# Kernel tuning notes

Hardware: AMD Instinct MI355X
Metric: run time of the kernel (lower is better)

The kernel has to match this reference:

```python
import jax, jax.numpy as jnp
import numpy as np

R_CUT = 10.0
ROUNDS = 1  # num_message_passing_rounds


def setup_inputs() -> dict:
    key = jax.random.key(0)
    N, DEG, S, NRBF, G = 10000, 16, 128, 20, 64
    E = N * DEG
    ks = jax.random.split(key, 16)
    w = lambda k, shp, fan: (jax.random.normal(k, shp, dtype=jnp.float32) / np.float32(np.sqrt(fan)))
    return {
        "edge_vector_diffs": jax.random.normal(ks[0], (E, 3), dtype=jnp.float32) * 3.0,
        "edge_lengths": jax.random.uniform(ks[1], (E,), dtype=jnp.float32) * 15.0,
        "node_from": jnp.repeat(jnp.arange(N), DEG),            # every node has DEG outgoing edges
        "node_graph_index": jax.random.randint(ks[2], (N,), 0, G),
        "num_graphs": G,
        "emb0": jax.random.normal(ks[3], (S,), dtype=jnp.float32) * 0.01,  # embedding.weight[0]
        "phi_w1": w(ks[4], (S, S), S), "phi_b1": jnp.zeros((S,), jnp.float32),
        "phi_w2": w(ks[5], (S, 3 * S), S), "phi_b2": jnp.zeros((3 * S,), jnp.float32),
        "filt_w": w(ks[6], (NRBF, 3 * S), NRBF), "filt_b": jnp.zeros((3 * S,), jnp.float32),
        "u_w": w(ks[7], (S, S), S), "v_w": w(ks[8], (S, S), S),
        "upd_w1": w(ks[9], (2 * S, S), 2 * S), "upd_b1": jnp.zeros((S,), jnp.float32),
        "upd_w2": w(ks[10], (S, 3 * S), S), "upd_b2": jnp.zeros((3 * S,), jnp.float32),
        "out_w1": w(ks[11], (S, S), S), "out_b1": jnp.zeros((S,), jnp.float32),
        "out_w2": w(ks[12], (S, 1), S), "out_b2": jnp.zeros((1,), jnp.float32),
    }


def reference(edge_vector_diffs, edge_lengths, node_from, node_graph_index, num_graphs,
              emb0, phi_w1, phi_b1, phi_w2, phi_b2, filt_w, filt_b, u_w, v_w,
              upd_w1, upd_b1, upd_w2, upd_b2, out_w1, out_b1, out_w2, out_b2):
    S = phi_w1.shape[0]
    N = node_graph_index.shape[0]
    NRBF = filt_w.shape[0]
    silu = jax.nn.silu
    seg = lambda v, n: jax.ops.segment_sum(v, node_from, num_segments=n)

    mask = (jnp.abs(edge_lengths) <= R_CUT).astype(jnp.float32)          # [E] nbr_mask
    r = jnp.linalg.norm(edge_vector_diffs, axis=1)                        # [E]
    r_safe = jnp.maximum(r, 1e-12)
    k = jnp.arange(1, NRBF + 1, dtype=jnp.float32)
    # PAINN sinc radial basis sin(k*pi*r/r_cut)/r, then linear -> [E, 3S]
    rbf = jnp.sin(k[None, :] * jnp.pi * r_safe[:, None] / R_CUT) / r_safe[:, None]
    cutoff = 0.5 * (jnp.cos(jnp.pi * r / R_CUT) + 1.0) * (r < R_CUT)      # cosine cutoff
    W = (rbf @ filt_w + filt_b) * cutoff[:, None]                          # [E, 3S]

    tile3 = jnp.arange(S) % 3  # xyzxyz... truncation pattern from .repeat(...)[: S]
    # scalar Frobenius norm of each node's masked neighbor-diff block
    frob = jnp.sqrt(seg(mask * r * r, N))                                  # [N]
    denom_e = frob[node_from]
    denom_e = jnp.where(denom_e > 0, denom_e, 1.0)
    normalized = edge_vector_diffs / denom_e[:, None]                      # [E, 3]
    norm_exp = normalized[:, tile3]                                        # [E, S]

    # state init: sum over dim 1 of embedding(zeros) == S * embedding.weight[0]
    state = jnp.broadcast_to(jnp.float32(S) * emb0, (N, S))
    state_vec = jnp.zeros((N, 3, S), jnp.float32)

    for _ in range(ROUNDS):
        # message block (nbrs_node_from == destination node, so sync update == original sequential loop)
        phi = silu(state[node_from] @ phi_w1 + phi_b1) @ phi_w2 + phi_b2   # [E, 3S]
        prod = phi * W
        m1, m2, m3 = prod[:, :S], prod[:, S:2 * S], prod[:, 2 * S:]
        vec_msg = state_vec[node_from] * m1[:, None, :] + (norm_exp * m3)[:, None, :]  # [E,3,S]
        state = seg(m2 * mask[:, None], N)                                 # [N, S]
        state_vec = seg(vec_msg * mask[:, None, None], N)                  # [N, 3, S]
        # update block
        U = jnp.einsum('nps,st->npt', state_vec, u_w)                      # [N,3,S]
        V = jnp.einsum('nps,st->npt', state_vec, v_w)
        UV = jnp.einsum('nps,nqs->npq', U, V)                              # [N,3,3]
        Vnorm = jnp.sqrt(jnp.sum(V * V, axis=1))                           # [N,S]
        a = silu(jnp.concatenate([Vnorm, state], axis=-1) @ upd_w1 + upd_b1) @ upd_w2 + upd_b2
        a_vv, a_sv, a_ss = a[:, :S], a[:, S:2 * S], a[:, 2 * S:]
        uv_tiled = jnp.sum(UV, axis=1)[:, tile3]                           # [N,S]
        state = a_ss + uv_tiled * a_sv
        state_vec = U * a_vv[:, None, :]

    graph_state = jax.ops.segment_sum(state, node_graph_index, num_segments=num_graphs)
    out = (silu(graph_state @ out_w1 + out_b1) @ out_w2 + out_b2).ravel()  # [num_graphs]
    return out
```

## Files before the change

### kernel.cpp

```cpp
#include <hip/hip_runtime.h>
#include <math.h>

#define NN   10000
#define DEG  16
#define SS   128
#define NRBF 20
#define GG   64
#define RC   10.0f
#define PI_F 3.14159265358979323846f
#define NB   4

__device__ __forceinline__ float silu_f(float x){
    return x / (1.0f + __expf(-x));
}

__global__ __launch_bounds__(128) void k_phi(
    const float* __restrict__ emb0,
    const float* __restrict__ w1, const float* __restrict__ b1,
    const float* __restrict__ w2, const float* __restrict__ b2,
    float* __restrict__ phiW){
    __shared__ float s0[SS];
    __shared__ float hL[SS];
    __shared__ float part[2][4];
    int t = threadIdx.x, bid = blockIdx.x;
    s0[t] = 128.0f * emb0[t];
    __syncthreads();
    float acc = 0.0f;
    #pragma unroll 8
    for (int s = 0; s < SS; s++)
        acc = fmaf(s0[s], w1[s*SS + t], acc);
    hL[t] = silu_f(acc + b1[t]);
    __syncthreads();
    int c0 = bid * 4;
    float4 wq = *((const float4*)(w2 + t*3*SS + c0));
    float h = hL[t];
    float p[4] = {h*wq.x, h*wq.y, h*wq.z, h*wq.w};
    int lane = t & 63, wid = t >> 6;
    #pragma unroll
    for (int j = 0; j < 4; j++){
        float v = p[j];
        for (int off = 32; off; off >>= 1) v += __shfl_down(v, off);
        if (lane == 0) part[wid][j] = v;
    }
    __syncthreads();
    if (t < 4) phiW[c0 + t] = b2[c0 + t] + part[0][t] + part[1][t];
}

__global__ __launch_bounds__(128) void k_node(
    const float* __restrict__ evd, const float* __restrict__ elen,
    const float* __restrict__ filt_w, const float* __restrict__ filt_b,
    const float* __restrict__ phiW,
    const float* __restrict__ u_w, const float* __restrict__ v_w,
    const float* __restrict__ upd_w1, const float* __restrict__ upd_b1,
    const float* __restrict__ upd_w2, const float* __restrict__ upd_b2,
    const int* __restrict__ ngi, float* __restrict__ gs){
    __shared__ float rS[NB*DEG];
    __shared__ float mcL[NB*DEG];
    __shared__ float frL[NB*DEG];
    __shared__ float eV[NB*DEG][3];
    __shared__ float rbfL[NB*DEG][NRBF];
    __shared__ float invD[NB];
    __shared__ float gsum[NB][4][NRBF+1];
    __shared__ __align__(16) float svT[SS][NB];
    __shared__ __align__(16) float xT[2*SS][NB];
    __shared__ __align__(16) float h2T[SS][NB];
    __shared__ float red[2][NB];
    __shared__ float dL[NB];
    int t  = threadIdx.x;
    int n0 = blockIdx.x * NB;

    if (t < NB*DEG){
        int e = n0*DEG + t;
        float x = evd[3*e+0], y = evd[3*e+1], z = evd[3*e+2];
        float r = sqrtf(x*x + y*y + z*z);
        float len  = elen[e];
        float mask = (fabsf(len) <= RC) ? 1.0f : 0.0f;
        float cut  = (r < RC) ? 0.5f*(cosf(PI_F*r*(1.0f/RC)) + 1.0f) : 0.0f;
        rS[t]  = fmaxf(r, 1e-12f);
        mcL[t] = mask * cut;
        frL[t] = mask * r * r;
        eV[t][0] = x; eV[t][1] = y; eV[t][2] = z;
    }
    __syncthreads();
    for (int idx = t; idx < NB*DEG*NRBF; idx += 128){
        int e = idx / NRBF, k = idx % NRBF;
        float rs = rS[e];
        rbfL[e][k] = sinf((float)(k+1) * (PI_F/RC) * rs) / rs;
    }
    if (t < NB){
        float s = 0.0f;
        for (int j = 0; j < DEG; j++) s += frL[t*DEG + j];
        float fbn = sqrtf(s);
        invD[t] = (fbn > 0.0f) ? 1.0f/fbn : 1.0f;
    }
    __syncthreads();

    for (int idx = t; idx < NB*4*(NRBF+1); idx += 128){
        int n   = idx / (4*(NRBF+1));
        int rem = idx % (4*(NRBF+1));
        int q   = rem / (NRBF+1);
        int k   = rem % (NRBF+1);
        float s = 0.0f;
        #pragma unroll
        for (int e = 0; e < DEG; e++){
            int ee = n*DEG + e;
            float w = mcL[ee];
            if (q > 0) w *= eV[ee][q-1];
            float rb = (k < NRBF) ? rbfL[ee][k] : 1.0f;
            s = fmaf(w, rb, s);
        }
        gsum[n][q][k] = s;
    }
    __syncthreads();

    {
        int gc1 = SS + t;
        int gc2 = 2*SS + t;
        float fw1[NRBF], fw2[NRBF];
        #pragma unroll
        for (int k = 0; k < NRBF; k++){
            fw1[k] = filt_w[k*(3*SS) + gc1];
            fw2[k] = filt_w[k*(3*SS) + gc2];
        }
        float fb1 = filt_b[gc1], fb2 = filt_b[gc2];
        float ph1 = phiW[gc1],   ph2 = phiW[gc2];
        int   s3  = t % 3;

        #pragma unroll
        for (int b = 0; b < NB; b++){
            float a1 = fb1 * gsum[b][0][NRBF];
            float a2 = fb2 * gsum[b][s3+1][NRBF];
            #pragma unroll
            for (int k = 0; k < NRBF; k++){
                a1 = fmaf(gsum[b][0][k],    fw1[k], a1);
                a2 = fmaf(gsum[b][s3+1][k], fw2[k], a2);
            }
            svT[t][b]   = ph2 * invD[b] * a2;
            xT[SS+t][b] = ph1 * a1;
        }
    }
    __syncthreads();

    float accU[NB], accV[NB];
    #pragma unroll
    for (int b = 0; b < NB; b++){ accU[b]=0.f; accV[b]=0.f; }
    for (int s = 0; s < SS; s++){
        float wu = u_w[s*SS + t];
        float wv = v_w[s*SS + t];
        float4 s03 = *((const float4*)(&svT[s][0]));
        float svv[NB] = {s03.x,s03.y,s03.z,s03.w};
        #pragma unroll
        for (int b = 0; b < NB; b++){
            accU[b] = fmaf(svv[b], wu, accU[b]);
            accV[b] = fmaf(svv[b], wv, accV[b]);
        }
    }

    int lane = t & 63, wid = t >> 6;
    #pragma unroll
    for (int b = 0; b < NB; b++){
        float p = accU[b]*accV[b];
        for (int off = 32; off; off >>= 1) p += __shfl_down(p, off);
        if (lane == 0) red[wid][b] = p;
    }
    {
        float4 q0;
        q0.x = sqrtf(3.f*accV[0]*accV[0]); q0.y = sqrtf(3.f*accV[1]*accV[1]);
        q0.z = sqrtf(3.f*accV[2]*accV[2]); q0.w = sqrtf(3.f*accV[3]*accV[3]);
        ((float4*)(&xT[t][0]))[0] = q0;
    }
    __syncthreads();
    if (t < NB) dL[t] = red[0][t] + red[1][t];

    float accH[NB];
    #pragma unroll
    for (int b = 0; b < NB; b++) accH[b] = 0.f;
    for (int i = 0; i < 2*SS; i++){
        float w = upd_w1[i*SS + t];
        float4 x03 = *((const float4*)(&xT[i][0]));
        float xv[NB] = {x03.x,x03.y,x03.z,x03.w};
        #pragma unroll
        for (int b = 0; b < NB; b++) accH[b] = fmaf(xv[b], w, accH[b]);
    }
    float b1v = upd_b1[t];
    {
        float4 q0;
        q0.x = silu_f(accH[0]+b1v); q0.y = silu_f(accH[1]+b1v);
        q0.z = silu_f(accH[2]+b1v); q0.w = silu_f(accH[3]+b1v);
        ((float4*)(&h2T[t][0]))[0] = q0;
    }
    __syncthreads();

    float a1[NB], a2[NB];
    #pragma unroll
    for (int b = 0; b < NB; b++){ a1[b]=0.f; a2[b]=0.f; }
    for (int j = 0; j < SS; j++){
        float w1 = upd_w2[j*3*SS + SS   + t];
        float w2 = upd_w2[j*3*SS + 2*SS + t];
        float4 h03 = *((const float4*)(&h2T[j][0]));
        float hv[NB] = {h03.x,h03.y,h03.z,h03.w};
        #pragma unroll
        for (int b = 0; b < NB; b++){
            a1[b] = fmaf(hv[b], w1, a1[b]);
            a2[b] = fmaf(hv[b], w2, a2[b]);
        }
    }
    float bsv = upd_b2[SS+t], bss = upd_b2[2*SS+t];
    #pragma unroll
    for (int b = 0; b < NB; b++){
        float ns = (a2[b] + bss) + 3.0f*dL[b]*(a1[b] + bsv);
        int g = ngi[n0+b];
        atomicAdd(&gs[g*SS + t], ns);
    }
}

__global__ __launch_bounds__(128) void k_out(
    const float* __restrict__ gs,
    const float* __restrict__ w1, const float* __restrict__ b1,
    const float* __restrict__ w2, const float* __restrict__ b2,
    float* __restrict__ out){
    __shared__ float gsL[SS];
    __shared__ float red[2];
    int g = blockIdx.x, t = threadIdx.x;
    gsL[t] = gs[g*SS + t];
    __syncthreads();
    float acc = b1[t];
    #pragma unroll 4
    for (int s = 0; s < SS; s++) acc = fmaf(gsL[s], w1[s*SS + t], acc);
    float p = silu_f(acc) * w2[t];
    for (int off = 32; off; off >>= 1) p += __shfl_down(p, off);
    if ((t & 63) == 0) red[t >> 6] = p;
    __syncthreads();
    if (t == 0) out[g] = red[0] + red[1] + b2[0];
}

extern "C" void kernel_launch(void* const* d_in, const int* in_sizes, int n_in,
                              void* d_out, int out_size, void* d_ws, size_t ws_size,
                              hipStream_t stream) {
    const float* evd     = (const float*)d_in[0];
    const float* elen    = (const float*)d_in[1];
    const int*   ngi     = (const int*)  d_in[3];
    const float* emb0    = (const float*)d_in[5];
    const float* phi_w1  = (const float*)d_in[6];
    const float* phi_b1  = (const float*)d_in[7];
    const float* phi_w2  = (const float*)d_in[8];
    const float* phi_b2  = (const float*)d_in[9];
    const float* filt_w  = (const float*)d_in[10];
    const float* filt_b  = (const float*)d_in[11];
    const float* u_w     = (const float*)d_in[12];
    const float* v_w     = (const float*)d_in[13];
    const float* upd_w1  = (const float*)d_in[14];
    const float* upd_b1  = (const float*)d_in[15];
    const float* upd_w2  = (const float*)d_in[16];
    const float* upd_b2  = (const float*)d_in[17];
    const float* out_w1  = (const float*)d_in[18];
    const float* out_b1  = (const float*)d_in[19];
    const float* out_w2  = (const float*)d_in[20];
    const float* out_b2  = (const float*)d_in[21];

    float* ws    = (float*)d_ws;
    float* phiW  = ws;
    float* gs    = ws + 512;

    hipMemsetAsync(gs, 0, GG*SS*sizeof(float), stream);
    k_phi<<<96, 128, 0, stream>>>(emb0, phi_w1, phi_b1, phi_w2, phi_b2, phiW);
    k_node<<<NN/NB, 128, 0, stream>>>(evd, elen, filt_w, filt_b, phiW,
                                      u_w, v_w, upd_w1, upd_b1, upd_w2, upd_b2,
                                      ngi, gs);
    k_out<<<GG, 128, 0, stream>>>(gs, out_w1, out_b1, out_w2, out_b2, (float*)d_out);
}
```

Measured before the change: 174.1 us.

## Split node-kernel matvecs across four thread groups with shared-memory partial reduction

Raises k_node from 128 to 512 threads per block. Each 128-thread group takes a quarter of the reduction dimension in the U/V, update-layer-1 and update-layer-2 matvecs and writes partial sums to shared memory, which are then combined per node. The filter step gives each group one node. The aim is to cut the serial loop length per thread and add latency hiding for the many weight loads, at the cost of extra barriers, shared-memory traffic and a larger shared footprint that may limit blocks per CU.

New measurement: 171.4 us. Within noise of the previous version (-1.5%).

```diff
diff --git a/kernel.cpp b/kernel.cpp
--- a/kernel.cpp
+++ b/kernel.cpp
@@ -9,6 +9,7 @@
 #define RC   10.0f
 #define PI_F 3.14159265358979323846f
 #define NB   4
+#define TPB  512
 
 __device__ __forceinline__ float silu_f(float x){
     return x / (1.0f + __expf(-x));
@@ -46,7 +47,7 @@
     if (t < 4) phiW[c0 + t] = b2[c0 + t] + part[0][t] + part[1][t];
 }
 
-__global__ __launch_bounds__(128) void k_node(
+__global__ __launch_bounds__(512) void k_node(
     const float* __restrict__ evd, const float* __restrict__ elen,
     const float* __restrict__ filt_w, const float* __restrict__ filt_b,
     const float* __restrict__ phiW,
@@ -64,16 +65,20 @@
     __shared__ __align__(16) float svT[SS][NB];
     __shared__ __align__(16) float xT[2*SS][NB];
     __shared__ __align__(16) float h2T[SS][NB];
-    __shared__ float red[2][NB];
+    __shared__ __align__(16) float part[4][SS][8];
+    __shared__ float red2[4][2];
     __shared__ float dL[NB];
-    int t  = threadIdx.x;
-    int n0 = blockIdx.x * NB;
+    int t    = threadIdx.x;
+    int ch   = t & 127;
+    int kk   = t >> 7;
+    int lane = t & 63, wid = t >> 6;
+    int n0   = blockIdx.x * NB;
 
     if (t < NB*DEG){
         int e = n0*DEG + t;
         float x = evd[3*e+0], y = evd[3*e+1], z = evd[3*e+2];
         float r = sqrtf(x*x + y*y + z*z);
-        float len  = elen[e];
+        float len  = elen[t + n0*DEG];
         float mask = (fabsf(len) <= RC) ? 1.0f : 0.0f;
         float cut  = (r < RC) ? 0.5f*(cosf(PI_F*r*(1.0f/RC)) + 1.0f) : 0.0f;
         rS[t]  = fmaxf(r, 1e-12f);
@@ -82,7 +87,7 @@
         eV[t][0] = x; eV[t][1] = y; eV[t][2] = z;
     }
     __syncthreads();
-    for (int idx = t; idx < NB*DEG*NRBF; idx += 128){
+    for (int idx = t; idx < NB*DEG*NRBF; idx += TPB){
         int e = idx / NRBF, k = idx % NRBF;
         float rs = rS[e];
         rbfL[e][k] = sinf((float)(k+1) * (PI_F/RC) * rs) / rs;
@@ -95,7 +100,7 @@
     }
     __syncthreads();
 
-    for (int idx = t; idx < NB*4*(NRBF+1); idx += 128){
+    for (int idx = t; idx < NB*4*(NRBF+1); idx += TPB){
         int n   = idx / (4*(NRBF+1));
         int rem = idx % (4*(NRBF+1));
         int q   = rem / (NRBF+1);
@@ -114,103 +119,103 @@
     __syncthreads();
 
     {
-        int gc1 = SS + t;
-        int gc2 = 2*SS + t;
-        float fw1[NRBF], fw2[NRBF];
+        int b   = kk;
+        int gc1 = SS + ch;
+        int gc2 = 2*SS + ch;
+        int s3  = ch % 3;
+        float a1 = filt_b[gc1] * gsum[b][0][NRBF];
+        float a2 = filt_b[gc2] * gsum[b][s3+1][NRBF];
         #pragma unroll
         for (int k = 0; k < NRBF; k++){
-            fw1[k] = filt_w[k*(3*SS) + gc1];
-            fw2[k] = filt_w[k*(3*SS) + gc2];
-        }
-        float fb1 = filt_b[gc1], fb2 = filt_b[gc2];
-        float ph1 = phiW[gc1],   ph2 = phiW[gc2];
-        int   s3  = t % 3;
-
-        #pragma unroll
-        for (int b = 0; b < NB; b++){
-            float a1 = fb1 * gsum[b][0][NRBF];
-            float a2 = fb2 * gsum[b][s3+1][NRBF];
+            a1 = fmaf(gsum[b][0][k],    filt_w[k*(3*SS) + gc1], a1);
+            a2 = fmaf(gsum[b][s3+1][k], filt_w[k*(3*SS) + gc2], a2);
+        }
+        svT[ch][b]   = phiW[gc2] * invD[b] * a2;
+        xT[SS+ch][b] = phiW[gc1] * a1;
+    }
+    __syncthreads();
+
+    {
+        float accU[NB], accV[NB];
+        #pragma unroll
+        for (int b = 0; b < NB; b++){ accU[b]=0.f; accV[b]=0.f; }
+        int sBeg = 32*kk;
+        for (int s = sBeg; s < sBeg+32; s++){
+            float wu = u_w[s*SS + ch];
+            float wv = v_w[s*SS + ch];
+            float4 s03 = *((const float4*)(&svT[s][0]));
+            float svv[NB] = {s03.x,s03.y,s03.z,s03.w};
             #pragma unroll
-            for (int k = 0; k < NRBF; k++){
-                a1 = fmaf(gsum[b][0][k],    fw1[k], a1);
-                a2 = fmaf(gsum[b][s3+1][k], fw2[k], a2);
+            for (int b = 0; b < NB; b++){
+                accU[b] = fmaf(svv[b], wu, accU[b]);
+                accV[b] = fmaf(svv[b], wv, accV[b]);
             }
-            svT[t][b]   = ph2 * invD[b] * a2;
-            xT[SS+t][b] = ph1 * a1;
-        }
-    }
-    __syncthreads();
-
-    float accU[NB], accV[NB];
-    #pragma unroll
-    for (int b = 0; b < NB; b++){ accU[b]=0.f; accV[b]=0.f; }
-    for (int s = 0; s < SS; s++){
-        float wu = u_w[s*SS + t];
-        float wv = v_w[s*SS + t];
-        float4 s03 = *((const float4*)(&svT[s][0]));
-        float svv[NB] = {s03.x,s03.y,s03.z,s03.w};
-        #pragma unroll
-        for (int b = 0; b < NB; b++){
-            accU[b] = fmaf(svv[b], wu, accU[b]);
-            accV[b] = fmaf(svv[b], wv, accV[b]);
-        }
-    }
-
-    int lane = t & 63, wid = t >> 6;
-    #pragma unroll
-    for (int b = 0; b < NB; b++){
-        float p = accU[b]*accV[b];
+        }
+        *((float4*)(&part[kk][ch][0])) = make_float4(accU[0],accU[1],accU[2],accU[3]);
+        *((float4*)(&part[kk][ch][4])) = make_float4(accV[0],accV[1],accV[2],accV[3]);
+    }
+    __syncthreads();
+    {
+        int b = kk;
+        float U = part[0][ch][b]   + part[1][ch][b]   + part[2][ch][b]   + part[3][ch][b];
+        float V = part[0][ch][4+b] + part[1][ch][4+b] + part[2][ch][4+b] + part[3][ch][4+b];
+        float p = U*V;
         for (int off = 32; off; off >>= 1) p += __shfl_down(p, off);
-        if (lane == 0) red[wid][b] = p;
-    }
-    {
-        float4 q0;
-        q0.x = sqrtf(3.f*accV[0]*accV[0]); q0.y = sqrtf(3.f*accV[1]*accV[1]);
-        q0.z = sqrtf(3.f*accV[2]*accV[2]); q0.w = sqrtf(3.f*accV[3]*accV[3]);
-        ((float4*)(&xT[t][0]))[0] = q0;
-    }
-    __syncthreads();
-    if (t < NB) dL[t] = red[0][t] + red[1][t];
-
-    float accH[NB];
-    #pragma unroll
-    for (int b = 0; b < NB; b++) accH[b] = 0.f;
-    for (int i = 0; i < 2*SS; i++){
-        float w = upd_w1[i*SS + t];
-        float4 x03 = *((const float4*)(&xT[i][0]));
-        float xv[NB] = {x03.x,x03.y,x03.z,x03.w};
-        #pragma unroll
-        for (int b = 0; b < NB; b++) accH[b] = fmaf(xv[b], w, accH[b]);
-    }
-    float b1v = upd_b1[t];
-    {
-        float4 q0;
-        q0.x = silu_f(accH[0]+b1v); q0.y = silu_f(accH[1]+b1v);
-        q0.z = silu_f(accH[2]+b1v); q0.w = silu_f(accH[3]+b1v);
-        ((float4*)(&h2T[t][0]))[0] = q0;
-    }
-    __syncthreads();
-
-    float a1[NB], a2[NB];
-    #pragma unroll
-    for (int b = 0; b < NB; b++){ a1[b]=0.f; a2[b]=0.f; }
-    for (int j = 0; j < SS; j++){
-        float w1 = upd_w2[j*3*SS + SS   + t];
-        float w2 = upd_w2[j*3*SS + 2*SS + t];
-        float4 h03 = *((const float4*)(&h2T[j][0]));
-        float hv[NB] = {h03.x,h03.y,h03.z,h03.w};
-        #pragma unroll
-        for (int b = 0; b < NB; b++){
-            a1[b] = fmaf(hv[b], w1, a1[b]);
-            a2[b] = fmaf(hv[b], w2, a2[b]);
-        }
-    }
-    float bsv = upd_b2[SS+t], bss = upd_b2[2*SS+t];
-    #pragma unroll
-    for (int b = 0; b < NB; b++){
-        float ns = (a2[b] + bss) + 3.0f*dL[b]*(a1[b] + bsv);
-        int g = ngi[n0+b];
-        atomicAdd(&gs[g*SS + t], ns);
+        if (lane == 0) red2[kk][wid & 1] = p;
+        xT[ch][b] = sqrtf(3.f*V*V);
+    }
+    __syncthreads();
+    if (t < NB) dL[t] = red2[t][0] + red2[t][1];
+
+    {
+        float accH[NB];
+        #pragma unroll
+        for (int b = 0; b < NB; b++) accH[b] = 0.f;
+        int iBeg = 64*kk;
+        for (int i = iBeg; i < iBeg+64; i++){
+            float w = upd_w1[i*SS + ch];
+            float4 x03 = *((const float4*)(&xT[i][0]));
+            float xv[NB] = {x03.x,x03.y,x03.z,x03.w};
+            #pragma unroll
+            for (int b = 0; b < NB; b++) accH[b] = fmaf(xv[b], w, accH[b]);
+        }
+        *((float4*)(&part[kk][ch][0])) = make_float4(accH[0],accH[1],accH[2],accH[3]);
+    }
+    __syncthreads();
+    {
+        int b = kk;
+        float H = part[0][ch][b] + part[1][ch][b] + part[2][ch][b] + part[3][ch][b];
+        h2T[ch][b] = silu_f(H + upd_b1[ch]);
+    }
+    __syncthreads();
+
+    {
+        float a1[NB], a2[NB];
+        #pragma unroll
+        for (int b = 0; b < NB; b++){ a1[b]=0.f; a2[b]=0.f; }
+        int jBeg = 32*kk;
+        for (int j = jBeg; j < jBeg+32; j++){
+            float w1 = upd_w2[j*3*SS + SS   + ch];
+            float w2 = upd_w2[j*3*SS + 2*SS + ch];
+            float4 h03 = *((const float4*)(&h2T[j][0]));
+            float hv[NB] = {h03.x,h03.y,h03.z,h03.w};
+            #pragma unroll
+            for (int b = 0; b < NB; b++){
+                a1[b] = fmaf(hv[b], w1, a1[b]);
+                a2[b] = fmaf(hv[b], w2, a2[b]);
+            }
+        }
+        *((float4*)(&part[kk][ch][0])) = make_float4(a1[0],a1[1],a1[2],a1[3]);
+        *((float4*)(&part[kk][ch][4])) = make_float4(a2[0],a2[1],a2[2],a2[3]);
+    }
+    __syncthreads();
+    {
+        int b = kk;
+        float A1 = part[0][ch][b]   + part[1][ch][b]   + part[2][ch][b]   + part[3][ch][b];
+        float A2 = part[0][ch][4+b] + part[1][ch][4+b] + part[2][ch][4+b] + part[3][ch][4+b];
+        float ns = (A2 + upd_b2[2*SS+ch]) + 3.0f*dL[b]*(A1 + upd_b2[SS+ch]);
+        int g = ngi[n0 + b];
+        atomicAdd(&gs[g*SS + ch], ns);
     }
 }
 
@@ -264,7 +269,7 @@
 
     hipMemsetAsync(gs, 0, GG*SS*sizeof(float), stream);
     k_phi<<<96, 128, 0, stream>>>(emb0, phi_w1, phi_b1, phi_w2, phi_b2, phiW);
-    k_node<<<NN/NB, 128, 0, stream>>>(evd, elen, filt_w, filt_b, phiW,
+    k_node<<<NN/NB, TPB, 0, stream>>>(evd, elen, filt_w, filt_b, phiW,
                                       u_w, v_w, upd_w1, upd_b1, upd_w2, upd_b2,
                                       ngi, gs);
     k_out<<<GG, 128, 0, stream>>>(gs, out_w1, out_b1, out_w2, out_b2, (float*)d_out);
```
